# Optimization experiments

Measured on AMD Instinct MI355X. Metric: run time of the kernel, lower is better.

Reference implementation:

```python
import jax, jax.numpy as jnp
import numpy as np

BETA = 0.9
ADAPT_RATE = 0.1


def _surrogate_spike(x):
    gate = jax.nn.sigmoid(5.0 * x)
    hard = (x > 0).astype(x.dtype)
    return jax.lax.stop_gradient(hard - gate) + gate


def setup_inputs() -> dict:
    key = jax.random.key(0)
    k1, k2, k3, k4, k5 = jax.random.split(key, 5)
    B, T, D, H = 64, 256, 512, 1024
    x = jax.random.normal(k1, (B, T, D), dtype=jnp.float32)
    # fc_in: Linear(D, H); fc_out: Linear(H, 1)
    W_in = jax.random.normal(k2, (H, D), dtype=jnp.float32) * (1.0 / np.sqrt(D))
    b_in = jax.random.normal(k3, (H,), dtype=jnp.float32) * 0.01
    W_out = jax.random.normal(k4, (1, H), dtype=jnp.float32) * (1.0 / np.sqrt(H))
    b_out = jax.random.normal(k5, (1,), dtype=jnp.float32) * 0.01
    return {"x": x, "W_in": W_in, "b_in": b_in, "W_out": W_out, "b_out": b_out}


def reference(x, W_in, b_in, W_out, b_out):
    B, T, D = x.shape
    H = W_in.shape[0]
    # batch fc_in over all timesteps outside the recurrence
    pre = jnp.einsum('btd,hd->bth', x, W_in) + b_in  # [B,T,H]

    def step(carry, p_t):
        mem, adapt = carry
        mem = BETA * mem + p_t - adapt
        spk = _surrogate_spike(mem)
        adapt = adapt + ADAPT_RATE * spk
        mem = mem - spk  # reset_mode == 'subtract'
        return (mem, adapt), spk

    init = (jnp.zeros((B, H), x.dtype), jnp.zeros((B, H), x.dtype))
    _, spks = jax.lax.scan(step, init, jnp.swapaxes(pre, 0, 1))  # spks: [T,B,H]

    # mean_t fc_out(spk_t) == fc_out(mean_t spk_t) since fc_out is affine
    spk_mean = spks.mean(axis=0)  # [B,H]
    return spk_mean @ W_out.T + b_out  # [B,1]
```

## Files before the change

### kernel.cpp

```cpp
#include <hip/hip_runtime.h>

constexpr int Bb = 64;
constexpr int Tt = 256;
constexpr int Dd = 512;
constexpr int Hh = 1024;
constexpr int Mm = Bb * Tt;

typedef _Float16 half8 __attribute__((ext_vector_type(8)));
typedef _Float16 half4v __attribute__((ext_vector_type(4)));
typedef float floatx16 __attribute__((ext_vector_type(16)));

#define GPTR(x) ((const __attribute__((address_space(1))) void*)(x))
#define LPTR(x) ((__attribute__((address_space(3))) void*)(x))

__global__ __launch_bounds__(256) void convert_t(const float* __restrict__ x,
                                                 const float* __restrict__ Win,
                                                 _Float16* __restrict__ xh,
                                                 _Float16* __restrict__ xl,
                                                 _Float16* __restrict__ wh,
                                                 _Float16* __restrict__ wl) {
    __shared__ _Float16 lh[64 * 72];
    __shared__ _Float16 ll[64 * 72];
    const int tid = threadIdx.x;
    const int k0 = blockIdx.x * 64;

    const float* src;
    _Float16 *dh, *dl;
    int nrows, m0;
    if (blockIdx.y < 256) {
        src = x; dh = xh; dl = xl; nrows = Mm; m0 = blockIdx.y * 64;
    } else {
        src = Win; dh = wh; dl = wl; nrows = Hh; m0 = (blockIdx.y - 256) * 64;
    }

#pragma unroll
    for (int i = 0; i < 4; ++i) {
        const int lin = tid + i * 256;
        const int row = lin >> 4;
        const int c4 = (lin & 15) * 4;
        const float4 v = *(const float4*)(src + (size_t)(m0 + row) * Dd + k0 + c4);
        const float va[4] = {v.x, v.y, v.z, v.w};
        half4v h, l;
#pragma unroll
        for (int q = 0; q < 4; ++q) {
            const _Float16 hi = (_Float16)va[q];
            h[q] = hi;
            l[q] = (_Float16)((va[q] - (float)hi) * 4096.0f);
        }
        *(half4v*)&lh[row * 72 + c4] = h;
        *(half4v*)&ll[row * 72 + c4] = l;
    }
    __syncthreads();
#pragma unroll
    for (int i = 0; i < 2; ++i) {
        const int lin = tid + i * 256;
        const int kc = lin >> 6;
        const int mm = lin & 63;
        const half8 h = *(const half8*)&lh[mm * 72 + kc * 8];
        const half8 l = *(const half8*)&ll[mm * 72 + kc * 8];
        const size_t g = (size_t)(k0 / 8 + kc) * nrows + m0 + mm;
        *(half8*)(dh + g * 8) = h;
        *(half8*)(dl + g * 8) = l;
    }
}

__global__ __launch_bounds__(256) void gemm_f16x2(const _Float16* __restrict__ xh,
                                                  const _Float16* __restrict__ xl,
                                                  const _Float16* __restrict__ wh,
                                                  const _Float16* __restrict__ wl,
                                                  const float* __restrict__ bin,
                                                  float* __restrict__ pre) {
    __shared__ _Float16 lds[2][4][4096];

    const int tid = threadIdx.x;
    const int m0 = blockIdx.y * 128;
    const int n0 = blockIdx.x * 128;
    const int lane = tid & 63;
    const int wave = tid >> 6;
    const int wm = (wave & 1) * 64;
    const int wn = (wave >> 1) * 64;
    const int lr = lane & 31;
    const int lk = lane >> 5;

    floatx16 acc[2][2], accx[2][2];
#pragma unroll
    for (int mi = 0; mi < 2; ++mi)
#pragma unroll
        for (int ni = 0; ni < 2; ++ni)
#pragma unroll
            for (int r = 0; r < 16; ++r) { acc[mi][ni][r] = 0.0f; accx[mi][ni][r] = 0.0f; }

#define STAGE(buf, kc0)                                                              \
    do {                                                                             \
        _Pragma("unroll")                                                            \
        for (int i_ = 0; i_ < 2; ++i_) {                                             \
            const int c_ = tid + i_ * 256;                                           \
            const int kp_ = c_ >> 7;                                                 \
            const int row_ = c_ & 127;                                               \
            const size_t ga_ = ((size_t)((kc0) + kp_) * Mm + m0 + row_) * 8;         \
            const size_t gb_ = ((size_t)((kc0) + kp_) * Hh + n0 + row_) * 8;         \
            __builtin_amdgcn_global_load_lds(GPTR(xh + ga_), LPTR(&lds[buf][0][c_ * 8]), 16, 0, 0); \
            __builtin_amdgcn_global_load_lds(GPTR(xl + ga_), LPTR(&lds[buf][1][c_ * 8]), 16, 0, 0); \
            __builtin_amdgcn_global_load_lds(GPTR(wh + gb_), LPTR(&lds[buf][2][c_ * 8]), 16, 0, 0); \
            __builtin_amdgcn_global_load_lds(GPTR(wl + gb_), LPTR(&lds[buf][3][c_ * 8]), 16, 0, 0); \
        }                                                                            \
    } while (0)

    STAGE(0, 0);

    for (int s = 0; s < 16; ++s) {
        __syncthreads();
        if (s < 15) STAGE((s + 1) & 1, (s + 1) * 4);
        const int cur = s & 1;
#pragma unroll
        for (int s2 = 0; s2 < 2; ++s2) {
            half8 ah[2], al[2], bh[2], bl[2];
#pragma unroll
            for (int mi = 0; mi < 2; ++mi) {
                const int ci = (s2 * 2 + lk) * 128 + wm + mi * 32 + lr;
                ah[mi] = *(const half8*)&lds[cur][0][ci * 8];
                al[mi] = *(const half8*)&lds[cur][1][ci * 8];
            }
#pragma unroll
            for (int ni = 0; ni < 2; ++ni) {
                const int ci = (s2 * 2 + lk) * 128 + wn + ni * 32 + lr;
                bh[ni] = *(const half8*)&lds[cur][2][ci * 8];
                bl[ni] = *(const half8*)&lds[cur][3][ci * 8];
            }
#pragma unroll
            for (int mi = 0; mi < 2; ++mi)
#pragma unroll
                for (int ni = 0; ni < 2; ++ni) {
                    acc[mi][ni]  = __builtin_amdgcn_mfma_f32_32x32x16_f16(ah[mi], bh[ni], acc[mi][ni], 0, 0, 0);
                    accx[mi][ni] = __builtin_amdgcn_mfma_f32_32x32x16_f16(ah[mi], bl[ni], accx[mi][ni], 0, 0, 0);
                    accx[mi][ni] = __builtin_amdgcn_mfma_f32_32x32x16_f16(al[mi], bh[ni], accx[mi][ni], 0, 0, 0);
                }
        }
    }
#undef STAGE

    const float bv0 = bin[n0 + wn + lr];
    const float bv1 = bin[n0 + wn + 32 + lr];
#pragma unroll
    for (int mi = 0; mi < 2; ++mi)
#pragma unroll
        for (int ni = 0; ni < 2; ++ni) {
            const float bv = ni ? bv1 : bv0;
#pragma unroll
            for (int r = 0; r < 16; ++r) {
                const int row = (r & 3) + 8 * (r >> 2) + 4 * lk;
                const int m = m0 + wm + mi * 32 + row;
                const int n = n0 + wn + ni * 32 + lr;
                pre[(size_t)m * Hh + n] =
                    acc[mi][ni][r] + accx[mi][ni][r] * (1.0f / 4096.0f) + bv;
            }
        }
}

#define BK 16
#define BMP 132
__global__ __launch_bounds__(256) void gemm_pre(const float* __restrict__ x,
                                                const float* __restrict__ Win,
                                                const float* __restrict__ bin,
                                                float* __restrict__ pre) {
    __shared__ float As[BK][BMP];
    __shared__ float Bs[BK][BMP];
    const int tid = threadIdx.x;
    const int m0 = blockIdx.y * 128;
    const int n0 = blockIdx.x * 128;
    const int tx = tid & 15;
    const int ty = tid >> 4;
    float acc[8][8];
#pragma unroll
    for (int i = 0; i < 8; ++i)
#pragma unroll
        for (int j = 0; j < 8; ++j) acc[i][j] = 0.0f;
    const float* Aptr = x + (size_t)m0 * Dd;
    const float* Bptr = Win + (size_t)n0 * Dd;
    for (int k0 = 0; k0 < Dd; k0 += BK) {
#pragma unroll
        for (int i = 0; i < 2; ++i) {
            const int lin = tid + i * 256;
            const int row = lin >> 2;
            const int kq = (lin & 3) << 2;
            const float4 av = *(const float4*)(Aptr + (size_t)row * Dd + k0 + kq);
            const float4 bv = *(const float4*)(Bptr + (size_t)row * Dd + k0 + kq);
            As[kq + 0][row] = av.x; As[kq + 1][row] = av.y;
            As[kq + 2][row] = av.z; As[kq + 3][row] = av.w;
            Bs[kq + 0][row] = bv.x; Bs[kq + 1][row] = bv.y;
            Bs[kq + 2][row] = bv.z; Bs[kq + 3][row] = bv.w;
        }
        __syncthreads();
#pragma unroll
        for (int kk = 0; kk < BK; ++kk) {
            const float4 a0 = *(const float4*)&As[kk][ty * 4];
            const float4 a1 = *(const float4*)&As[kk][ty * 4 + 64];
            const float4 b0 = *(const float4*)&Bs[kk][tx * 4];
            const float4 b1 = *(const float4*)&Bs[kk][tx * 4 + 64];
            const float a[8] = {a0.x, a0.y, a0.z, a0.w, a1.x, a1.y, a1.z, a1.w};
            const float b[8] = {b0.x, b0.y, b0.z, b0.w, b1.x, b1.y, b1.z, b1.w};
#pragma unroll
            for (int i = 0; i < 8; ++i)
#pragma unroll
                for (int j = 0; j < 8; ++j) acc[i][j] += a[i] * b[j];
        }
        __syncthreads();
    }
#pragma unroll
    for (int i = 0; i < 8; ++i) {
        const int m = m0 + ((i < 4) ? (ty * 4 + i) : (64 + ty * 4 + i - 4));
#pragma unroll
        for (int half = 0; half < 2; ++half) {
            const int n = n0 + tx * 4 + half * 64;
            float4 v;
            v.x = acc[i][half * 4 + 0] + bin[n + 0];
            v.y = acc[i][half * 4 + 1] + bin[n + 1];
            v.z = acc[i][half * 4 + 2] + bin[n + 2];
            v.w = acc[i][half * 4 + 3] + bin[n + 3];
            *(float4*)(pre + (size_t)m * Hh + n) = v;
        }
    }
}

__global__ __launch_bounds__(256) void alif_scan(const float* __restrict__ pre,
                                                 const float* __restrict__ Wout,
                                                 float* __restrict__ partials) {
    const int h = blockIdx.x * 256 + threadIdx.x;
    const int b = blockIdx.y;
    const float* p = pre + (size_t)b * Tt * Hh + h;

    float buf[32];
#pragma unroll
    for (int j = 0; j < 32; ++j) buf[j] = p[(size_t)j * Hh];

    float mem = 0.0f, adapt = 0.0f, cnt = 0.0f;
    for (int t0 = 0; t0 < Tt; t0 += 32) {
        float cur[32];
#pragma unroll
        for (int j = 0; j < 32; ++j) cur[j] = buf[j];
        if (t0 + 32 < Tt) {
#pragma unroll
            for (int j = 0; j < 32; ++j) buf[j] = p[(size_t)(t0 + 32 + j) * Hh];
        }
#pragma unroll
        for (int j = 0; j < 32; ++j) {
            mem = 0.9f * mem + cur[j] - adapt;
            const float spk = (mem > 0.0f) ? 1.0f : 0.0f;
            adapt += 0.1f * spk;
            mem -= spk;
            cnt += spk;
        }
    }

    __shared__ float red[256];
    red[threadIdx.x] = cnt * Wout[h];
    __syncthreads();
#pragma unroll
    for (int s = 128; s > 0; s >>= 1) {
        if (threadIdx.x < s) red[threadIdx.x] += red[threadIdx.x + s];
        __syncthreads();
    }
    if (threadIdx.x == 0) partials[b * gridDim.x + blockIdx.x] = red[0];
}

__global__ void finalize(const float* __restrict__ partials,
                         const float* __restrict__ bout,
                         float* __restrict__ out, int nchunks) {
    const int b = threadIdx.x;
    float s = 0.0f;
    for (int c = 0; c < nchunks; ++c) s += partials[b * nchunks + c];
    out[b] = s * (1.0f / (float)Tt) + bout[0];
}

extern "C" void kernel_launch(void* const* d_in, const int* in_sizes, int n_in,
                              void* d_out, int out_size, void* d_ws, size_t ws_size,
                              hipStream_t stream) {
    const float* x    = (const float*)d_in[0];
    const float* Win  = (const float*)d_in[1];
    const float* bin  = (const float*)d_in[2];
    const float* Wout = (const float*)d_in[3];
    const float* bout = (const float*)d_in[4];
    float* out = (float*)d_out;

    const size_t pre_bytes = (size_t)Mm * Hh * 4;
    const size_t xh_bytes  = (size_t)Mm * Dd * 2;
    const size_t wh_bytes  = (size_t)Hh * Dd * 2;
    float* pre = (float*)d_ws;

    const size_t need = pre_bytes + 2 * xh_bytes + 2 * wh_bytes + 4096;
    if (ws_size >= need) {
        char* base = (char*)d_ws + pre_bytes;
        _Float16* xh = (_Float16*)base;
        _Float16* xl = (_Float16*)(base + xh_bytes);
        _Float16* wh = (_Float16*)(base + 2 * xh_bytes);
        _Float16* wl = (_Float16*)(base + 2 * xh_bytes + wh_bytes);
        float* partials = (float*)(base + 2 * xh_bytes + 2 * wh_bytes);

        convert_t<<<dim3(8, 272), 256, 0, stream>>>(x, Win, xh, xl, wh, wl);

        dim3 g1(Hh / 128, Mm / 128);
        gemm_f16x2<<<g1, 256, 0, stream>>>(xh, xl, wh, wl, bin, pre);

        dim3 g2(Hh / 256, Bb);
        alif_scan<<<g2, 256, 0, stream>>>(pre, Wout, partials);
        finalize<<<1, 64, 0, stream>>>(partials, bout, out, Hh / 256);
    } else {
        float* partials = (float*)((char*)d_ws + pre_bytes);
        dim3 g1(Hh / 128, Mm / 128);
        gemm_pre<<<g1, 256, 0, stream>>>(x, Win, bin, pre);
        dim3 g2(Hh / 256, Bb);
        alif_scan<<<g2, 256, 0, stream>>>(pre, Wout, partials);
        finalize<<<1, 64, 0, stream>>>(partials, bout, out, Hh / 256);
    }
}
```

Measured before the change: 157.0 us.

## Fuse finalize into scan via atomics and swizzle GEMM block order

The separate finalize kernel is removed. The output is now initialized with the bias inside the convert kernel, and the scan does a wave-level shuffle reduction followed by an atomicAdd into the output, which saves a launch and the partials buffer. The scan now runs with 64-thread blocks, giving more blocks per batch. The GEMM grid becomes 1D with a swizzled tile mapping that groups 8 M-tiles per column sweep, meant to improve L2 reuse of the activation tiles. Atomic accumulation makes the summation order nondeterministic.

```diff
diff --git a/kernel.cpp b/kernel.cpp
--- a/kernel.cpp
+++ b/kernel.cpp
@@ -18,11 +18,15 @@
                                                  _Float16* __restrict__ xh,
                                                  _Float16* __restrict__ xl,
                                                  _Float16* __restrict__ wh,
-                                                 _Float16* __restrict__ wl) {
+                                                 _Float16* __restrict__ wl,
+                                                 const float* __restrict__ bout,
+                                                 float* __restrict__ out) {
     __shared__ _Float16 lh[64 * 72];
     __shared__ _Float16 ll[64 * 72];
     const int tid = threadIdx.x;
     const int k0 = blockIdx.x * 64;
+
+    if (blockIdx.x == 0 && blockIdx.y == 0 && tid < Bb) out[tid] = bout[0];
 
     const float* src;
     _Float16 *dh, *dl;
@@ -73,8 +77,12 @@
     __shared__ _Float16 lds[2][4][4096];
 
     const int tid = threadIdx.x;
-    const int m0 = blockIdx.y * 128;
-    const int n0 = blockIdx.x * 128;
+    const int id = blockIdx.x;
+    const int j  = id & 7;
+    const int s  = id >> 3;
+    const int m0 = (((s >> 3) << 3) | j) * 128;
+    const int n0 = (s & 7) * 128;
+
     const int lane = tid & 63;
     const int wave = tid >> 6;
     const int wm = (wave & 1) * 64;
@@ -108,10 +116,10 @@
 
     STAGE(0, 0);
 
-    for (int s = 0; s < 16; ++s) {
+    for (int ss = 0; ss < 16; ++ss) {
         __syncthreads();
-        if (s < 15) STAGE((s + 1) & 1, (s + 1) * 4);
-        const int cur = s & 1;
+        if (ss < 15) STAGE((ss + 1) & 1, (ss + 1) * 4);
+        const int cur = ss & 1;
 #pragma unroll
         for (int s2 = 0; s2 < 2; ++s2) {
             half8 ah[2], al[2], bh[2], bl[2];
@@ -174,7 +182,7 @@
 #pragma unroll
     for (int i = 0; i < 8; ++i)
 #pragma unroll
-        for (int j = 0; j < 8; ++j) acc[i][j] = 0.0f;
+        for (int jj = 0; jj < 8; ++jj) acc[i][jj] = 0.0f;
     const float* Aptr = x + (size_t)m0 * Dd;
     const float* Bptr = Win + (size_t)n0 * Dd;
     for (int k0 = 0; k0 < Dd; k0 += BK) {
@@ -202,7 +210,7 @@
 #pragma unroll
             for (int i = 0; i < 8; ++i)
 #pragma unroll
-                for (int j = 0; j < 8; ++j) acc[i][j] += a[i] * b[j];
+                for (int jj = 0; jj < 8; ++jj) acc[i][jj] += a[i] * b[jj];
         }
         __syncthreads();
     }
@@ -222,29 +230,34 @@
     }
 }
 
-__global__ __launch_bounds__(256) void alif_scan(const float* __restrict__ pre,
-                                                 const float* __restrict__ Wout,
-                                                 float* __restrict__ partials) {
-    const int h = blockIdx.x * 256 + threadIdx.x;
+__global__ __launch_bounds__(64) void init_out(const float* __restrict__ bout,
+                                               float* __restrict__ out) {
+    out[threadIdx.x] = bout[0];
+}
+
+__global__ __launch_bounds__(64) void alif_scan(const float* __restrict__ pre,
+                                                const float* __restrict__ Wout,
+                                                float* __restrict__ out) {
+    const int h = blockIdx.x * 64 + threadIdx.x;
     const int b = blockIdx.y;
     const float* p = pre + (size_t)b * Tt * Hh + h;
 
     float buf[32];
 #pragma unroll
-    for (int j = 0; j < 32; ++j) buf[j] = p[(size_t)j * Hh];
+    for (int jj = 0; jj < 32; ++jj) buf[jj] = p[(size_t)jj * Hh];
 
     float mem = 0.0f, adapt = 0.0f, cnt = 0.0f;
     for (int t0 = 0; t0 < Tt; t0 += 32) {
         float cur[32];
 #pragma unroll
-        for (int j = 0; j < 32; ++j) cur[j] = buf[j];
+        for (int jj = 0; jj < 32; ++jj) cur[jj] = buf[jj];
         if (t0 + 32 < Tt) {
 #pragma unroll
-            for (int j = 0; j < 32; ++j) buf[j] = p[(size_t)(t0 + 32 + j) * Hh];
-        }
-#pragma unroll
-        for (int j = 0; j < 32; ++j) {
-            mem = 0.9f * mem + cur[j] - adapt;
+            for (int jj = 0; jj < 32; ++jj) buf[jj] = p[(size_t)(t0 + 32 + jj) * Hh];
+        }
+#pragma unroll
+        for (int jj = 0; jj < 32; ++jj) {
+            mem = 0.9f * mem + cur[jj] - adapt;
             const float spk = (mem > 0.0f) ? 1.0f : 0.0f;
             adapt += 0.1f * spk;
             mem -= spk;
@@ -252,24 +265,10 @@
         }
     }
 
-    __shared__ float red[256];
-    red[threadIdx.x] = cnt * Wout[h];
-    __syncthreads();
-#pragma unroll
-    for (int s = 128; s > 0; s >>= 1) {
-        if (threadIdx.x < s) red[threadIdx.x] += red[threadIdx.x + s];
-        __syncthreads();
-    }
-    if (threadIdx.x == 0) partials[b * gridDim.x + blockIdx.x] = red[0];
-}
-
-__global__ void finalize(const float* __restrict__ partials,
-                         const float* __restrict__ bout,
-                         float* __restrict__ out, int nchunks) {
-    const int b = threadIdx.x;
-    float s = 0.0f;
-    for (int c = 0; c < nchunks; ++c) s += partials[b * nchunks + c];
-    out[b] = s * (1.0f / (float)Tt) + bout[0];
+    float val = cnt * Wout[h] * (1.0f / (float)Tt);
+#pragma unroll
+    for (int off = 32; off > 0; off >>= 1) val += __shfl_down(val, off, 64);
+    if (threadIdx.x == 0) atomicAdd(&out[b], val);
 }
 
 extern "C" void kernel_launch(void* const* d_in, const int* in_sizes, int n_in,
@@ -294,22 +293,16 @@
         _Float16* xl = (_Float16*)(base + xh_bytes);
         _Float16* wh = (_Float16*)(base + 2 * xh_bytes);
         _Float16* wl = (_Float16*)(base + 2 * xh_bytes + wh_bytes);
-        float* partials = (float*)(base + 2 * xh_bytes + 2 * wh_bytes);
-
-        convert_t<<<dim3(8, 272), 256, 0, stream>>>(x, Win, xh, xl, wh, wl);
-
-        dim3 g1(Hh / 128, Mm / 128);
-        gemm_f16x2<<<g1, 256, 0, stream>>>(xh, xl, wh, wl, bin, pre);
-
-        dim3 g2(Hh / 256, Bb);
-        alif_scan<<<g2, 256, 0, stream>>>(pre, Wout, partials);
-        finalize<<<1, 64, 0, stream>>>(partials, bout, out, Hh / 256);
+
+        convert_t<<<dim3(8, 272), 256, 0, stream>>>(x, Win, xh, xl, wh, wl, bout, out);
+
+        gemm_f16x2<<<1024, 256, 0, stream>>>(xh, xl, wh, wl, bin, pre);
+
+        alif_scan<<<dim3(Hh / 64, Bb), 64, 0, stream>>>(pre, Wout, out);
     } else {
-        float* partials = (float*)((char*)d_ws + pre_bytes);
+        init_out<<<1, 64, 0, stream>>>(bout, out);
         dim3 g1(Hh / 128, Mm / 128);
         gemm_pre<<<g1, 256, 0, stream>>>(x, Win, bin, pre);
-        dim3 g2(Hh / 256, Bb);
-        alif_scan<<<g2, 256, 0, stream>>>(pre, Wout, partials);
-        finalize<<<1, 64, 0, stream>>>(partials, bout, out, Hh / 256);
-    }
-}
+        alif_scan<<<dim3(Hh / 64, Bb), 64, 0, stream>>>(pre, Wout, out);
+    }
+}
```

New measurement: 152.0 us. 3.2% less time.
